# Performance work log

Hardware: AMD Instinct MI355X
Metric: run time of the kernel (lower is better)

The kernel has to match this reference:

```python
import jax, jax.numpy as jnp
import numpy as np

B, S, D_MODEL, D_K, D_V, H = 2, 2048, 1024, 1024, 1024, 16


def setup_inputs() -> dict:
    key = jax.random.key(0)
    ks = jax.random.split(key, 12)
    s = 0.02
    inp = {
        "queries": jax.random.normal(ks[0], (B, S, D_MODEL), jnp.float32),
        "keys": jax.random.normal(ks[1], (B, S, D_MODEL), jnp.float32),
        "values": jax.random.normal(ks[2], (B, S, D_MODEL), jnp.float32),
        # causal mask: 1 where attention is disallowed (added as -1e9*mask)
        "mask": jnp.triu(jnp.ones((1, 1, S, S), jnp.float32), k=1),
        "Wq": jax.random.normal(ks[3], (D_MODEL, D_K), jnp.float32) * s,
        "bq": jnp.zeros((D_K,), jnp.float32),
        "Wk": jax.random.normal(ks[4], (D_MODEL, D_K), jnp.float32) * s,
        "bk": jnp.zeros((D_K,), jnp.float32),
        "Wv": jax.random.normal(ks[5], (D_MODEL, D_V), jnp.float32) * s,
        "bv": jnp.zeros((D_V,), jnp.float32),
        "Wo": jax.random.normal(ks[6], (D_K, D_MODEL), jnp.float32) * s,
        "bo": jnp.zeros((D_MODEL,), jnp.float32),
    }
    return inp


def _split_heads(x):  # [B,S,D] -> [B,H,S,D/H]
    b, s, d = x.shape
    return x.reshape(b, s, H, d // H).transpose(0, 2, 1, 3)


def reference(queries, keys, values, mask, Wq, bq, Wk, bk, Wv, bv, Wo, bo):
    q = _split_heads(queries @ Wq + bq)   # [B,H,S,hd]
    k = _split_heads(keys @ Wk + bk)
    v = _split_heads(values @ Wv + bv)
    # NOTE: original scales by sqrt(full d_k), not per-head dim (faithful quirk)
    scores = jnp.einsum("bhqd,bhkd->bhqk", q, k) / jnp.sqrt(jnp.float32(D_K))
    scores = scores + (-1e9) * mask
    w = jax.nn.softmax(scores, axis=-1)
    out = jnp.einsum("bhqk,bhkd->bhqd", w, v)        # [B,H,S,hd]
    out = out.transpose(0, 2, 1, 3).reshape(q.shape[0], q.shape[2], D_K)
    return out @ Wo + bo
```

## Files before the change

### kernel.cpp

```cpp
#include <hip/hip_runtime.h>
#include <hip/hip_bf16.h>
#include <cstdint>

typedef __bf16 bf16;
typedef __bf16 bf16x2 __attribute__((ext_vector_type(2)));
typedef __bf16 bf16x4 __attribute__((ext_vector_type(4)));
typedef __bf16 bf16x8 __attribute__((ext_vector_type(8)));
typedef float f32x4 __attribute__((ext_vector_type(4)));
typedef float f32x16 __attribute__((ext_vector_type(16)));
typedef unsigned int u32;

#define B_ 2
#define S_ 2048
#define DM 1024
#define H_ 16
#define HD 64

__device__ __forceinline__ void gload_lds16(const bf16* g, bf16* l) {
  __builtin_amdgcn_global_load_lds((const __attribute__((address_space(1))) void*)g,
                                   (__attribute__((address_space(3))) void*)l,
                                   16, 0, 0);
}

__device__ __forceinline__ u32 cvt_pk_bf16(float lo, float hi) {
  u32 r;
  asm("v_cvt_pk_bf16_f32 %0, %1, %2" : "=v"(r) : "v"(lo), "v"(hi));
  return r;
}

__global__ __launch_bounds__(256) void convert_k(const float* __restrict__ s0,
                                                 const float* __restrict__ s1,
                                                 const float* __restrict__ s2,
                                                 bf16* __restrict__ d0,
                                                 bf16* __restrict__ d1,
                                                 bf16* __restrict__ d2) {
  const float* s = (blockIdx.z == 0) ? s0 : (blockIdx.z == 1) ? s1 : s2;
  bf16* d = (blockIdx.z == 0) ? d0 : (blockIdx.z == 1) ? d1 : d2;
  const size_t i = ((size_t)blockIdx.x * 256 + threadIdx.x) * 8;
  f32x4 a = *(const f32x4*)(s + i);
  f32x4 b = *(const f32x4*)(s + i + 4);
  bf16x8 o;
#pragma unroll
  for (int j = 0; j < 4; j++) { o[j] = (bf16)a[j]; o[j + 4] = (bf16)b[j]; }
  *(bf16x8*)(d + i) = o;
}

__global__ __launch_bounds__(256) void transposeW_k(
    const float* __restrict__ w0, const float* __restrict__ w1,
    const float* __restrict__ w2, const float* __restrict__ w3,
    bf16* __restrict__ t0, bf16* __restrict__ t1,
    bf16* __restrict__ t2, bf16* __restrict__ t3) {
  const float* src = (blockIdx.z == 0) ? w0 : (blockIdx.z == 1) ? w1
                     : (blockIdx.z == 2) ? w2 : w3;
  bf16* dst = (blockIdx.z == 0) ? t0 : (blockIdx.z == 1) ? t1
              : (blockIdx.z == 2) ? t2 : t3;
  __shared__ float tile[32][33];
  const int tx = threadIdx.x, ty = threadIdx.y;
  const int x0 = blockIdx.x * 32, y0 = blockIdx.y * 32;
#pragma unroll
  for (int r = 0; r < 4; r++)
    tile[ty + r * 8][tx] = src[(size_t)(y0 + ty + r * 8) * DM + x0 + tx];
  __syncthreads();
#pragma unroll
  for (int r = 0; r < 4; r++)
    dst[(size_t)(x0 + ty + r * 8) * DM + y0 + tx] = (bf16)tile[tx][ty + r * 8];
}

struct GArgs { const void* A; const bf16* Bt; const float* bias; void* C; };
struct GArgs3 { GArgs g[3]; };

__global__ __launch_bounds__(512, 1) void gemm128_k(GArgs3 args, int M, int N,
                                                    int K) {
  __shared__ __align__(16) bf16 SA_[73728];
  bf16* const SB_ = SA_ + 24576;

  const int nwg = gridDim.x;
  const int id = blockIdx.x;
  const int wgid = (id & 7) * (nwg >> 3) + (id >> 3);
  const int z = wgid >> 7;
  const int rem = wgid & 127;
  const int tx = rem >> 5, ty = rem & 31;
  const GArgs ga = args.g[z];
  const int m0 = ty * 128, n0 = tx * 256;

  const int tid = threadIdx.x;
  const int lane = tid & 63, w = tid >> 6;
  const int l15 = lane & 15, q = lane >> 4;
  const int wr = w >> 2, wc = w & 3;

  const bf16* gA[2];
  const bf16* gB[4];
  int dA[2], dB[4];
#pragma unroll
  for (int i = 0; i < 2; i++) {
    const int ci = i * 512 + w * 64 + lane;
    const int row = ci >> 3, sc = (ci & 7) ^ (row & 7);
    gA[i] = (const bf16*)ga.A + (size_t)(m0 + row) * K + sc * 8;
    dA[i] = (i * 512 + w * 64) * 8;
  }
#pragma unroll
  for (int i = 0; i < 4; i++) {
    const int ci = i * 512 + w * 64 + lane;
    const int row = ci >> 3, sc = (ci & 7) ^ (row & 7);
    gB[i] = ga.Bt + (size_t)(n0 + row) * K + sc * 8;
    dB[i] = (i * 512 + w * 64) * 8;
  }

  const int cA0 = (q ^ (l15 & 7)) * 8;
  const int cA1 = ((4 + q) ^ (l15 & 7)) * 8;

  f32x4 acc[4][4] = {};

  const int NT = K >> 6;

#pragma unroll
  for (int tt = 0; tt < 2; tt++) {
    bf16* Ab = SA_ + tt * 8192;
    bf16* Bb = SB_ + tt * 16384;
    const int k0 = tt * 64;
    gload_lds16(gA[0] + k0, Ab + dA[0]);
    gload_lds16(gA[1] + k0, Ab + dA[1]);
#pragma unroll
    for (int i = 0; i < 4; i++) gload_lds16(gB[i] + k0, Bb + dB[i]);
  }
  asm volatile("s_waitcnt vmcnt(6)" ::: "memory");
  __builtin_amdgcn_s_barrier();

  for (int t = 0; t < NT; ++t) {
    const int rb = t % 3;
    const int wb = (t + 2) % 3;
    const int kpre = ((t + 2 < NT) ? t + 2 : NT - 1) << 6;
    {
      bf16* Ab = SA_ + wb * 8192;
      bf16* Bb = SB_ + wb * 16384;
      gload_lds16(gA[0] + kpre, Ab + dA[0]);
      gload_lds16(gA[1] + kpre, Ab + dA[1]);
#pragma unroll
      for (int i = 0; i < 4; i++) gload_lds16(gB[i] + kpre, Bb + dB[i]);
    }

    const bf16* Ab = SA_ + rb * 8192;
    const bf16* Bb = SB_ + rb * 16384;
    bf16x8 a[4][2], b[4][2];
#pragma unroll
    for (int mt = 0; mt < 4; mt++) {
      const int ro = (wr * 64 + mt * 16 + l15) * 64;
      a[mt][0] = *(const bf16x8*)(Ab + ro + cA0);
      a[mt][1] = *(const bf16x8*)(Ab + ro + cA1);
    }
#pragma unroll
    for (int nt = 0; nt < 4; nt++) {
      const int ro = (wc * 64 + nt * 16 + l15) * 64;
      b[nt][0] = *(const bf16x8*)(Bb + ro + cA0);
      b[nt][1] = *(const bf16x8*)(Bb + ro + cA1);
    }

    __builtin_amdgcn_s_setprio(1);
#pragma unroll
    for (int mt = 0; mt < 4; mt++)
#pragma unroll
      for (int nt = 0; nt < 4; nt++)
#pragma unroll
        for (int kk = 0; kk < 2; kk++)
          acc[mt][nt] = __builtin_amdgcn_mfma_f32_16x16x32_bf16(
              a[mt][kk], b[nt][kk], acc[mt][nt], 0, 0, 0);
    __builtin_amdgcn_s_setprio(0);

    asm volatile("s_waitcnt vmcnt(6)" ::: "memory");
    __builtin_amdgcn_s_barrier();
  }

  asm volatile("s_waitcnt vmcnt(0)" ::: "memory");
  __builtin_amdgcn_s_barrier();

  bf16* Ws = SA_ + w * 4352;
#pragma unroll
  for (int nt = 0; nt < 4; nt++) {
    const float bv = ga.bias[n0 + wc * 64 + nt * 16 + l15];
#pragma unroll
    for (int mt = 0; mt < 4; mt++)
#pragma unroll
      for (int r = 0; r < 4; r++)
        Ws[(mt * 16 + q * 4 + r) * 68 + nt * 16 + l15] =
            (bf16)(acc[mt][nt][r] + bv);
  }
#pragma unroll
  for (int p = 0; p < 8; p++) {
    const int lr = p * 8 + (lane >> 3), c0 = (lane & 7) * 8;
    bf16x4 lo = *(const bf16x4*)(Ws + lr * 68 + c0);
    bf16x4 hi = *(const bf16x4*)(Ws + lr * 68 + c0 + 4);
    bf16x8 o;
#pragma unroll
    for (int j = 0; j < 4; j++) { o[j] = lo[j]; o[j + 4] = hi[j]; }
    *(bf16x8*)((bf16*)ga.C + (size_t)(m0 + wr * 64 + lr) * N + n0 + wc * 64 + c0) = o;
  }
}

__global__ __launch_bounds__(512, 1) void gemmo_k(const bf16* __restrict__ A,
                                                  const bf16* __restrict__ Bt,
                                                  const float* __restrict__ bias,
                                                  float* __restrict__ C,
                                                  int M, int N, int K) {
  __shared__ __align__(16) bf16 SA_[49152];
  bf16* const SB_ = SA_ + 24576;

  const int id = blockIdx.x;
  const int wgid = (id & 7) * 32 + (id >> 3);
  const int tx = wgid >> 5, ty = wgid & 31;
  const int m0 = ty * 128, n0 = tx * 128;

  const int tid = threadIdx.x;
  const int lane = tid & 63, w = tid >> 6;
  const int l15 = lane & 15, q = lane >> 4;
  const int wr = w >> 2, wc = w & 3;

  const bf16* gA[2];
  const bf16* gB[2];
  int dd[2];
#pragma unroll
  for (int i = 0; i < 2; i++) {
    const int ci = i * 512 + w * 64 + lane;
    const int row = ci >> 3, sc = (ci & 7) ^ (row & 7);
    gA[i] = A + (size_t)(m0 + row) * K + sc * 8;
    gB[i] = Bt + (size_t)(n0 + row) * K + sc * 8;
    dd[i] = ci * 8;
  }

  const int cA0 = (q ^ (l15 & 7)) * 8;
  const int cA1 = ((4 + q) ^ (l15 & 7)) * 8;

  f32x4 acc[4][2] = {};
  const int NT = K >> 6;

#pragma unroll
  for (int tt = 0; tt < 2; tt++) {
    const int k0 = tt * 64;
    gload_lds16(gA[0] + k0, SA_ + tt * 8192 + dd[0]);
    gload_lds16(gA[1] + k0, SA_ + tt * 8192 + dd[1]);
    gload_lds16(gB[0] + k0, SB_ + tt * 8192 + dd[0]);
    gload_lds16(gB[1] + k0, SB_ + tt * 8192 + dd[1]);
  }
  asm volatile("s_waitcnt vmcnt(4)" ::: "memory");
  __builtin_amdgcn_s_barrier();

  for (int t = 0; t < NT; ++t) {
    const int rb = t % 3;
    const int wb = (t + 2) % 3;
    const int kpre = ((t + 2 < NT) ? t + 2 : NT - 1) << 6;
    gload_lds16(gA[0] + kpre, SA_ + wb * 8192 + dd[0]);
    gload_lds16(gA[1] + kpre, SA_ + wb * 8192 + dd[1]);
    gload_lds16(gB[0] + kpre, SB_ + wb * 8192 + dd[0]);
    gload_lds16(gB[1] + kpre, SB_ + wb * 8192 + dd[1]);

    const bf16* Ab = SA_ + rb * 8192;
    const bf16* Bb = SB_ + rb * 8192;
    bf16x8 a[4][2], b[2][2];
#pragma unroll
    for (int mt = 0; mt < 4; mt++) {
      const int ro = (wr * 64 + mt * 16 + l15) * 64;
      a[mt][0] = *(const bf16x8*)(Ab + ro + cA0);
      a[mt][1] = *(const bf16x8*)(Ab + ro + cA1);
    }
#pragma unroll
    for (int nt = 0; nt < 2; nt++) {
      const int ro = (wc * 32 + nt * 16 + l15) * 64;
      b[nt][0] = *(const bf16x8*)(Bb + ro + cA0);
      b[nt][1] = *(const bf16x8*)(Bb + ro + cA1);
    }

    __builtin_amdgcn_s_setprio(1);
#pragma unroll
    for (int mt = 0; mt < 4; mt++)
#pragma unroll
      for (int nt = 0; nt < 2; nt++)
#pragma unroll
        for (int kk = 0; kk < 2; kk++)
          acc[mt][nt] = __builtin_amdgcn_mfma_f32_16x16x32_bf16(
              a[mt][kk], b[nt][kk], acc[mt][nt], 0, 0, 0);
    __builtin_amdgcn_s_setprio(0);

    asm volatile("s_waitcnt vmcnt(4)" ::: "memory");
    __builtin_amdgcn_s_barrier();
  }

  asm volatile("s_waitcnt vmcnt(0)" ::: "memory");
  __builtin_amdgcn_s_barrier();

  float* Ws = (float*)SA_ + w * 2304;
#pragma unroll
  for (int nt = 0; nt < 2; nt++) {
    const float bv = bias[n0 + wc * 32 + nt * 16 + l15];
#pragma unroll
    for (int mt = 0; mt < 4; mt++)
#pragma unroll
      for (int r = 0; r < 4; r++)
        Ws[(mt * 16 + q * 4 + r) * 36 + nt * 16 + l15] = acc[mt][nt][r] + bv;
  }
#pragma unroll
  for (int p = 0; p < 8; p++) {
    const int lr = p * 8 + (lane >> 3), c0 = (lane & 7) * 4;
    f32x4 v = *(const f32x4*)(Ws + lr * 36 + c0);
    *(f32x4*)(C + (size_t)(m0 + wr * 64 + lr) * N + n0 + wc * 32 + c0) = v;
  }
}

template <bool AF32, bool CF32>
__global__ __launch_bounds__(256) void gemm_k(GArgs3 args, int M, int N, int K) {
  const GArgs ga = args.g[blockIdx.z];
  __shared__ __align__(16) bf16 As[128 * 32];
  __shared__ __align__(16) bf16 Bs[128 * 32];
  const int tid = threadIdx.x;
  const int lane = tid & 63, w = tid >> 6;
  const int l15 = lane & 15, q = lane >> 4;
  const int wr = w >> 1, wc = w & 1;
  const int m0 = blockIdx.y * 128, n0 = blockIdx.x * 128;

  const int c0 = w * 128 + lane;
  const int c1 = c0 + 64;
  const int r0 = c0 >> 2, r1 = c1 >> 2, koff = (c0 & 3) * 8;
  const bf16* gB0 = ga.Bt + (size_t)(n0 + r0) * K + koff;
  const bf16* gB1 = ga.Bt + (size_t)(n0 + r1) * K + koff;
  bf16* lA0 = As + (w * 2 + 0) * 512;
  bf16* lA1 = As + (w * 2 + 1) * 512;
  bf16* lB0 = Bs + (w * 2 + 0) * 512;
  bf16* lB1 = Bs + (w * 2 + 1) * 512;

  const float* pA0 = nullptr;
  const float* pA1 = nullptr;
  f32x4 t00, t01, t10, t11;
  if constexpr (AF32) {
    const float* A = (const float*)ga.A;
    pA0 = A + (size_t)(m0 + r0) * K + koff;
    pA1 = A + (size_t)(m0 + r1) * K + koff;
    t00 = *(const f32x4*)pA0; t01 = *(const f32x4*)(pA0 + 4);
    t10 = *(const f32x4*)pA1; t11 = *(const f32x4*)(pA1 + 4);
  }

  f32x4 acc[4][4] = {};

  for (int k0 = 0; k0 < K; k0 += 32) {
    if constexpr (AF32) {
      bf16x8 va0, va1;
#pragma unroll
      for (int j = 0; j < 4; j++) {
        va0[j] = (bf16)t00[j]; va0[j + 4] = (bf16)t01[j];
        va1[j] = (bf16)t10[j]; va1[j + 4] = (bf16)t11[j];
      }
      *(bf16x8*)(lA0 + lane * 8) = va0;
      *(bf16x8*)(lA1 + lane * 8) = va1;
    } else {
      const bf16* A = (const bf16*)ga.A;
      gload_lds16(A + (size_t)(m0 + r0) * K + koff + k0, lA0);
      gload_lds16(A + (size_t)(m0 + r1) * K + koff + k0, lA1);
    }
    gload_lds16(gB0 + k0, lB0);
    gload_lds16(gB1 + k0, lB1);
    __syncthreads();

    bf16x8 a[4], b[4];
#pragma unroll
    for (int mt = 0; mt < 4; mt++)
      a[mt] = *(const bf16x8*)(As + (wr * 64 + mt * 16 + l15) * 32 + q * 8);
#pragma unroll
    for (int nt = 0; nt < 4; nt++)
      b[nt] = *(const bf16x8*)(Bs + (wc * 64 + nt * 16 + l15) * 32 + q * 8);

    if constexpr (AF32) {
      const int kn = (k0 + 32 < K) ? k0 + 32 : k0;
      t00 = *(const f32x4*)(pA0 + kn); t01 = *(const f32x4*)(pA0 + kn + 4);
      t10 = *(const f32x4*)(pA1 + kn); t11 = *(const f32x4*)(pA1 + kn + 4);
    }

#pragma unroll
    for (int mt = 0; mt < 4; mt++)
#pragma unroll
      for (int nt = 0; nt < 4; nt++)
        acc[mt][nt] = __builtin_amdgcn_mfma_f32_16x16x32_bf16(a[mt], b[nt],
                                                              acc[mt][nt], 0, 0, 0);
    __syncthreads();
  }

#pragma unroll
  for (int nt = 0; nt < 4; nt++) {
    const int col = n0 + wc * 64 + nt * 16 + l15;
    const float bv = ga.bias[col];
#pragma unroll
    for (int mt = 0; mt < 4; mt++) {
      const int row = m0 + wr * 64 + mt * 16 + q * 4;
#pragma unroll
      for (int r = 0; r < 4; r++) {
        const float val = acc[mt][nt][r] + bv;
        if constexpr (CF32)
          ((float*)ga.C)[(size_t)(row + r) * N + col] = val;
        else
          ((bf16*)ga.C)[(size_t)(row + r) * N + col] = (bf16)val;
      }
    }
  }
}

__global__ __launch_bounds__(512, 4) void attn_k(const bf16* __restrict__ Qp,
                                                 const bf16* __restrict__ Kp,
                                                 const bf16* __restrict__ Vp,
                                                 bf16* __restrict__ Op) {
  const int g = blockIdx.x;
  const int xcd = g & 7, s = g >> 3;
  const int gl = s & 3, tau = s >> 2;
  const int bh = xcd * 4 + gl;
  const int b = bh >> 4, h = bh & 15;
  const int xt = (tau < 8) ? tau : 23 - tau;
  const int i0 = xt * 128;
  const int NI = 2 * xt + 2;

  const int tid = threadIdx.x;
  const int lane = tid & 63, w = tid >> 6;
  const int l31 = lane & 31, hi = lane >> 5;
  const int qq = w >> 1, kh = w & 1;

  __shared__ __align__(16) char smem[33792];
  bf16 (*Ks)[64][64] = (bf16 (*)[64][64])smem;
  bf16 (*Vts)[64][64] = (bf16 (*)[64][64])(smem + 16384);

  const size_t headoff = (size_t)b * S_ * DM + h * HD;
  const bf16* Kb = Kp + headoff;
  const bf16* Vb = Vp + headoff;

  const int kr = tid >> 3, kcb = (tid & 7) * 8;
  const int cK = ((tid & 7) ^ (kr & 7)) * 8;
  const int d0 = (tid & 31) * 2, kq = (tid >> 5) * 4;
  const int cV0 = ((kq >> 3) ^ (d0 & 7)) * 8 + (kq & 7);
  const int cV1 = ((kq >> 3) ^ ((d0 + 1) & 7)) * 8 + (kq & 7);
  const float QSCALE = 0.04508422f;

  bf16x8 qreg[4];
  {
    const bf16* qb = Qp + headoff + (size_t)(i0 + qq * 32 + l31) * DM + hi * 8;
#pragma unroll
    for (int kk = 0; kk < 4; kk++) {
      bf16x8 v = *(const bf16x8*)(qb + kk * 16);
      bf16x8 o;
#pragma unroll
      for (int j = 0; j < 8; j++) o[j] = (bf16)((float)v[j] * QSCALE);
      qreg[kk] = o;
    }
  }

  bf16x8 kR = *(const bf16x8*)(Kb + (size_t)kr * DM + kcb);
  bf16x2 vR[4];
#pragma unroll
  for (int j = 0; j < 4; j++)
    vR[j] = *(const bf16x2*)(Vb + (size_t)(kq + j) * DM + d0);
  *(bf16x8*)&Ks[0][kr][cK] = kR;
  {
    bf16x4 vlo, vhi;
#pragma unroll
    for (int j = 0; j < 4; j++) { vlo[j] = vR[j][0]; vhi[j] = vR[j][1]; }
    *(bf16x4*)&Vts[0][d0][cV0] = vlo;
    *(bf16x4*)&Vts[0][d0 + 1][cV1] = vhi;
  }
  kR = *(const bf16x8*)(Kb + (size_t)(64 + kr) * DM + kcb);
#pragma unroll
  for (int j = 0; j < 4; j++)
    vR[j] = *(const bf16x2*)(Vb + (size_t)(64 + kq + j) * DM + d0);
  __syncthreads();

  f32x16 oacc0 = {}, oacc1 = {};
  float rsum = 0.f;
  int buf = 0;
  const int qbase = i0 + qq * 32;

  for (int t = 0; t < NI; ++t, buf ^= 1) {
    if (t + 1 < NI) {
      *(bf16x8*)&Ks[buf ^ 1][kr][cK] = kR;
      bf16x4 vlo, vhi;
#pragma unroll
      for (int j = 0; j < 4; j++) { vlo[j] = vR[j][0]; vhi[j] = vR[j][1]; }
      *(bf16x4*)&Vts[buf ^ 1][d0][cV0] = vlo;
      *(bf16x4*)&Vts[buf ^ 1][d0 + 1][cV1] = vhi;
    }
    if (t + 2 < NI) {
      const size_t jn = (size_t)(t + 2) * 64;
      kR = *(const bf16x8*)(Kb + (jn + kr) * DM + kcb);
#pragma unroll
      for (int j = 0; j < 4; j++)
        vR[j] = *(const bf16x2*)(Vb + (jn + kq + j) * DM + d0);
    }

    const int kbase = t * 64 + kh * 32;
    if (kbase <= qbase + 31) {
      f32x16 sa = {}, sb = {};
      __builtin_amdgcn_s_setprio(1);
#pragma unroll
      for (int kk = 0; kk < 2; kk++) {
        bf16x8 ka = *(const bf16x8*)
            &Ks[buf][kh * 32 + l31][((2 * kk + hi) ^ (l31 & 7)) * 8];
        sa = __builtin_amdgcn_mfma_f32_32x32x16_bf16(ka, qreg[kk], sa, 0, 0, 0);
      }
#pragma unroll
      for (int kk = 2; kk < 4; kk++) {
        bf16x8 ka = *(const bf16x8*)
            &Ks[buf][kh * 32 + l31][((2 * kk + hi) ^ (l31 & 7)) * 8];
        sb = __builtin_amdgcn_mfma_f32_32x32x16_bf16(ka, qreg[kk], sb, 0, 0, 0);
      }
      __builtin_amdgcn_s_setprio(0);

      float p[16];
      if (kbase + 31 > qbase) {
        const int qrl = qbase + l31;
#pragma unroll
        for (int r = 0; r < 16; r++) {
          const int keyl = kbase + (r & 3) + 8 * (r >> 2) + 4 * hi;
          p[r] = (keyl <= qrl) ? __builtin_amdgcn_exp2f(sa[r] + sb[r]) : 0.f;
        }
      } else {
#pragma unroll
        for (int r = 0; r < 16; r++)
          p[r] = __builtin_amdgcn_exp2f(sa[r] + sb[r]);
      }
      {
        float q0 = (p[0] + p[1]) + (p[2] + p[3]);
        float q1 = (p[4] + p[5]) + (p[6] + p[7]);
        float q2 = (p[8] + p[9]) + (p[10] + p[11]);
        float q3 = (p[12] + p[13]) + (p[14] + p[15]);
        rsum += (q0 + q1) + (q2 + q3);
      }

      u32 Aq[4][2];
#pragma unroll
      for (int t2 = 0; t2 < 4; t2++) {
        Aq[t2][0] = cvt_pk_bf16(p[4 * t2 + 0], p[4 * t2 + 1]);
        Aq[t2][1] = cvt_pk_bf16(p[4 * t2 + 2], p[4 * t2 + 3]);
      }
      bf16x8 pb[2];
#pragma unroll
      for (int s2 = 0; s2 < 2; s2++) {
        auto e0 = __builtin_amdgcn_permlane32_swap(Aq[2 * s2][0], Aq[2 * s2 + 1][0], false, false);
        auto e1 = __builtin_amdgcn_permlane32_swap(Aq[2 * s2][1], Aq[2 * s2 + 1][1], false, false);
        union { u32 u[4]; bf16x8 v; } cv;
        cv.u[0] = e0[0]; cv.u[1] = e1[0]; cv.u[2] = e0[1]; cv.u[3] = e1[1];
        pb[s2] = cv.v;
      }

      __builtin_amdgcn_s_setprio(1);
#pragma unroll
      for (int s2 = 0; s2 < 2; s2++) {
        const int cv = ((kh * 4 + s2 * 2 + hi) ^ (l31 & 7)) * 8;
        bf16x8 va0 = *(const bf16x8*)&Vts[buf][l31][cv];
        bf16x8 va1 = *(const bf16x8*)&Vts[buf][32 + l31][cv];
        oacc0 = __builtin_amdgcn_mfma_f32_32x32x16_bf16(va0, pb[s2], oacc0, 0, 0, 0);
        oacc1 = __builtin_amdgcn_mfma_f32_32x32x16_bf16(va1, pb[s2], oacc1, 0, 0, 0);
      }
      __builtin_amdgcn_s_setprio(0);
    }

    __syncthreads();
  }

  float rtot_w = rsum + __shfl_xor(rsum, 32);
  float* osum = (float*)smem;
  float* auxf = (float*)(smem + 32768);
  if (kh == 0) {
#pragma unroll
    for (int m = 0; m < 2; m++)
#pragma unroll
      for (int rq = 0; rq < 4; rq++) {
        f32x4 v4;
#pragma unroll
        for (int e = 0; e < 4; e++)
          v4[e] = m ? oacc1[rq * 4 + e] : oacc0[rq * 4 + e];
        *(f32x4*)(osum + qq * 2048 + (m * 4 + rq) * 256 + lane * 4) = v4;
      }
  }
  if (lane < 32) auxf[w * 32 + lane] = rtot_w;
  __syncthreads();
  if (kh == 1) {
#pragma unroll
    for (int m = 0; m < 2; m++)
#pragma unroll
      for (int rq = 0; rq < 4; rq++) {
        float* pp = osum + qq * 2048 + (m * 4 + rq) * 256 + lane * 4;
        f32x4 v4 = *(f32x4*)pp;
#pragma unroll
        for (int e = 0; e < 4; e++)
          v4[e] += m ? oacc1[rq * 4 + e] : oacc0[rq * 4 + e];
        *(f32x4*)pp = v4;
      }
  }
  __syncthreads();

  {
    const int q = tid >> 2, q31b = q & 31, qq2 = q >> 5;
    const float rtot = auxf[(qq2 * 2 + 0) * 32 + q31b] + auxf[(qq2 * 2 + 1) * 32 + q31b];
    const float rinv = 1.0f / rtot;
    const int dbase = (tid & 3) * 16;
    bf16* orow = Op + headoff + (size_t)(i0 + q) * DM + dbase;
#pragma unroll
    for (int gg = 0; gg < 2; gg++) {
      bf16x8 o8;
#pragma unroll
      for (int e = 0; e < 8; e++) {
        const int d = dbase + gg * 8 + e;
        const int base = (((d >> 5) << 2) | ((d >> 3) & 3)) * 256 +
                         (q31b + 32 * ((d >> 2) & 1)) * 4 + (d & 3);
        o8[e] = (bf16)(osum[qq2 * 2048 + base] * rinv);
      }
      *(bf16x8*)(orow + gg * 8) = o8;
    }
  }
}

extern "C" void kernel_launch(void* const* d_in, const int* in_sizes, int n_in,
                              void* d_out, int out_size, void* d_ws, size_t ws_size,
                              hipStream_t stream) {
  const float* q_in = (const float*)d_in[0];
  const float* k_in = (const float*)d_in[1];
  const float* v_in = (const float*)d_in[2];
  const float* Wq = (const float*)d_in[4];
  const float* bq = (const float*)d_in[5];
  const float* Wk = (const float*)d_in[6];
  const float* bk = (const float*)d_in[7];
  const float* Wv = (const float*)d_in[8];
  const float* bv = (const float*)d_in[9];
  const float* Wo = (const float*)d_in[10];
  const float* bo = (const float*)d_in[11];

  bf16* ws = (bf16*)d_ws;
  const size_t NQ = (size_t)B_ * S_ * DM;
  bf16* Qp = ws;
  bf16* Kp = ws + NQ;
  bf16* Vp = ws + 2 * NQ;
  bf16* WqT = ws + 3 * NQ;
  bf16* WkT = WqT + (size_t)DM * DM;
  bf16* WvT = WkT + (size_t)DM * DM;
  bf16* WoT = WvT + (size_t)DM * DM;
  bf16* qb = WoT + (size_t)DM * DM;
  bf16* kb = qb + NQ;
  bf16* vb = kb + NQ;

  const bool fast = ws_size >= (size_t)(28 * 1024 * 1024) * 2;

  transposeW_k<<<dim3(32, 32, 4), dim3(32, 8), 0, stream>>>(
      Wq, Wk, Wv, Wo, WqT, WkT, WvT, WoT);

  if (fast) {
    convert_k<<<dim3((B_ * S_ * DM) / (256 * 8), 1, 3), 256, 0, stream>>>(
        q_in, k_in, v_in, qb, kb, vb);
    GArgs3 g3;
    g3.g[0] = {qb, WqT, bq, Qp};
    g3.g[1] = {kb, WkT, bk, Kp};
    g3.g[2] = {vb, WvT, bv, Vp};
    gemm128_k<<<dim3(384), 512, 0, stream>>>(g3, B_ * S_, DM, DM);
  } else {
    GArgs3 g3;
    g3.g[0] = {q_in, WqT, bq, Qp};
    g3.g[1] = {k_in, WkT, bk, Kp};
    g3.g[2] = {v_in, WvT, bv, Vp};
    gemm_k<true, false><<<dim3(DM / 128, (B_ * S_) / 128, 3), 256, 0, stream>>>(
        g3, B_ * S_, DM, DM);
  }

  attn_k<<<dim3(512, 1, 1), 512, 0, stream>>>(Qp, Kp, Vp, Qp);

  gemmo_k<<<dim3(256), 512, 0, stream>>>(Qp, WoT, bo, (float*)d_out,
                                         B_ * S_, DM, DM);
}
```

Baseline: 216.6 us.

## Fuse fp32-to-bf16 input conversion into the QKV projection GEMM

Removes the separate convert_k pass that wrote bf16 copies of queries/keys/values. The GEMM now loads fp32 A tiles into registers three stages ahead, converts them to bf16 and stores them into swizzled LDS, while B keeps using direct global-to-LDS loads. This avoids a full read/write round trip of the activations and one launch, but doubles A global read bytes inside the GEMM and adds register pressure and VALU conversion work in the main loop. The fallback gemm_k path is deleted.

```diff
diff --git a/kernel.cpp b/kernel.cpp
--- a/kernel.cpp
+++ b/kernel.cpp
@@ -28,21 +28,11 @@
   return r;
 }
 
-__global__ __launch_bounds__(256) void convert_k(const float* __restrict__ s0,
-                                                 const float* __restrict__ s1,
-                                                 const float* __restrict__ s2,
-                                                 bf16* __restrict__ d0,
-                                                 bf16* __restrict__ d1,
-                                                 bf16* __restrict__ d2) {
-  const float* s = (blockIdx.z == 0) ? s0 : (blockIdx.z == 1) ? s1 : s2;
-  bf16* d = (blockIdx.z == 0) ? d0 : (blockIdx.z == 1) ? d1 : d2;
-  const size_t i = ((size_t)blockIdx.x * 256 + threadIdx.x) * 8;
-  f32x4 a = *(const f32x4*)(s + i);
-  f32x4 b = *(const f32x4*)(s + i + 4);
+__device__ __forceinline__ bf16x8 cvt8(f32x4 lo, f32x4 hi) {
   bf16x8 o;
 #pragma unroll
-  for (int j = 0; j < 4; j++) { o[j] = (bf16)a[j]; o[j + 4] = (bf16)b[j]; }
-  *(bf16x8*)(d + i) = o;
+  for (int j = 0; j < 4; j++) { o[j] = (bf16)lo[j]; o[j + 4] = (bf16)hi[j]; }
+  return o;
 }
 
 __global__ __launch_bounds__(256) void transposeW_k(
@@ -88,16 +78,17 @@
   const int l15 = lane & 15, q = lane >> 4;
   const int wr = w >> 2, wc = w & 3;
 
-  const bf16* gA[2];
-  const bf16* gB[4];
-  int dA[2], dB[4];
+  const float* gAf[2];
+  int dAwr[2];
 #pragma unroll
   for (int i = 0; i < 2; i++) {
     const int ci = i * 512 + w * 64 + lane;
     const int row = ci >> 3, sc = (ci & 7) ^ (row & 7);
-    gA[i] = (const bf16*)ga.A + (size_t)(m0 + row) * K + sc * 8;
-    dA[i] = (i * 512 + w * 64) * 8;
-  }
+    gAf[i] = (const float*)ga.A + (size_t)(m0 + row) * K + sc * 8;
+    dAwr[i] = ci * 8;
+  }
+  const bf16* gB[4];
+  int dB[4];
 #pragma unroll
   for (int i = 0; i < 4; i++) {
     const int ci = i * 512 + w * 64 + lane;
@@ -110,34 +101,43 @@
   const int cA1 = ((4 + q) ^ (l15 & 7)) * 8;
 
   f32x4 acc[4][4] = {};
-
   const int NT = K >> 6;
 
-#pragma unroll
-  for (int tt = 0; tt < 2; tt++) {
-    bf16* Ab = SA_ + tt * 8192;
-    bf16* Bb = SB_ + tt * 16384;
-    const int k0 = tt * 64;
-    gload_lds16(gA[0] + k0, Ab + dA[0]);
-    gload_lds16(gA[1] + k0, Ab + dA[1]);
-#pragma unroll
-    for (int i = 0; i < 4; i++) gload_lds16(gB[i] + k0, Bb + dB[i]);
-  }
-  asm volatile("s_waitcnt vmcnt(6)" ::: "memory");
+  f32x4 a0l = *(const f32x4*)(gAf[0]);
+  f32x4 a0h = *(const f32x4*)(gAf[0] + 4);
+  f32x4 a1l = *(const f32x4*)(gAf[1]);
+  f32x4 a1h = *(const f32x4*)(gAf[1] + 4);
+  f32x4 c0l = *(const f32x4*)(gAf[0] + 64);
+  f32x4 c0h = *(const f32x4*)(gAf[0] + 68);
+  f32x4 c1l = *(const f32x4*)(gAf[1] + 64);
+  f32x4 c1h = *(const f32x4*)(gAf[1] + 68);
+#pragma unroll
+  for (int i = 0; i < 4; i++) gload_lds16(gB[i], SB_ + dB[i]);
+  f32x4 p0l = *(const f32x4*)(gAf[0] + 128);
+  f32x4 p0h = *(const f32x4*)(gAf[0] + 132);
+  f32x4 p1l = *(const f32x4*)(gAf[1] + 128);
+  f32x4 p1h = *(const f32x4*)(gAf[1] + 132);
+#pragma unroll
+  for (int i = 0; i < 4; i++) gload_lds16(gB[i] + 64, SB_ + 16384 + dB[i]);
+  *(bf16x8*)(SA_ + dAwr[0]) = cvt8(a0l, a0h);
+  *(bf16x8*)(SA_ + dAwr[1]) = cvt8(a1l, a1h);
+  *(bf16x8*)(SA_ + 8192 + dAwr[0]) = cvt8(c0l, c0h);
+  *(bf16x8*)(SA_ + 8192 + dAwr[1]) = cvt8(c1l, c1h);
+  asm volatile("s_waitcnt vmcnt(8) lgkmcnt(0)" ::: "memory");
   __builtin_amdgcn_s_barrier();
 
   for (int t = 0; t < NT; ++t) {
     const int rb = t % 3;
-    const int wb = (t + 2) % 3;
-    const int kpre = ((t + 2 < NT) ? t + 2 : NT - 1) << 6;
-    {
-      bf16* Ab = SA_ + wb * 8192;
-      bf16* Bb = SB_ + wb * 16384;
-      gload_lds16(gA[0] + kpre, Ab + dA[0]);
-      gload_lds16(gA[1] + kpre, Ab + dA[1]);
-#pragma unroll
-      for (int i = 0; i < 4; i++) gload_lds16(gB[i] + kpre, Bb + dB[i]);
-    }
+    const int w2 = (t + 2) % 3;
+    *(bf16x8*)(SA_ + w2 * 8192 + dAwr[0]) = cvt8(p0l, p0h);
+    *(bf16x8*)(SA_ + w2 * 8192 + dAwr[1]) = cvt8(p1l, p1h);
+    const int ka = ((t + 3 < NT) ? t + 3 : NT - 1) << 6;
+    p0l = *(const f32x4*)(gAf[0] + ka); p0h = *(const f32x4*)(gAf[0] + ka + 4);
+    p1l = *(const f32x4*)(gAf[1] + ka); p1h = *(const f32x4*)(gAf[1] + ka + 4);
+    const int kb2 = ((t + 2 < NT) ? t + 2 : NT - 1) << 6;
+#pragma unroll
+    for (int i = 0; i < 4; i++)
+      gload_lds16(gB[i] + kb2, SB_ + w2 * 16384 + dB[i]);
 
     const bf16* Ab = SA_ + rb * 8192;
     const bf16* Bb = SB_ + rb * 16384;
@@ -154,7 +154,6 @@
       b[nt][0] = *(const bf16x8*)(Bb + ro + cA0);
       b[nt][1] = *(const bf16x8*)(Bb + ro + cA1);
     }
-
     __builtin_amdgcn_s_setprio(1);
 #pragma unroll
     for (int mt = 0; mt < 4; mt++)
@@ -166,11 +165,11 @@
               a[mt][kk], b[nt][kk], acc[mt][nt], 0, 0, 0);
     __builtin_amdgcn_s_setprio(0);
 
-    asm volatile("s_waitcnt vmcnt(6)" ::: "memory");
+    asm volatile("s_waitcnt vmcnt(8) lgkmcnt(0)" ::: "memory");
     __builtin_amdgcn_s_barrier();
   }
 
-  asm volatile("s_waitcnt vmcnt(0)" ::: "memory");
+  asm volatile("s_waitcnt vmcnt(0) lgkmcnt(0)" ::: "memory");
   __builtin_amdgcn_s_barrier();
 
   bf16* Ws = SA_ + w * 4352;
@@ -301,101 +300,6 @@
     const int lr = p * 8 + (lane >> 3), c0 = (lane & 7) * 4;
     f32x4 v = *(const f32x4*)(Ws + lr * 36 + c0);
     *(f32x4*)(C + (size_t)(m0 + wr * 64 + lr) * N + n0 + wc * 32 + c0) = v;
-  }
-}
-
-template <bool AF32, bool CF32>
-__global__ __launch_bounds__(256) void gemm_k(GArgs3 args, int M, int N, int K) {
-  const GArgs ga = args.g[blockIdx.z];
-  __shared__ __align__(16) bf16 As[128 * 32];
-  __shared__ __align__(16) bf16 Bs[128 * 32];
-  const int tid = threadIdx.x;
-  const int lane = tid & 63, w = tid >> 6;
-  const int l15 = lane & 15, q = lane >> 4;
-  const int wr = w >> 1, wc = w & 1;
-  const int m0 = blockIdx.y * 128, n0 = blockIdx.x * 128;
-
-  const int c0 = w * 128 + lane;
-  const int c1 = c0 + 64;
-  const int r0 = c0 >> 2, r1 = c1 >> 2, koff = (c0 & 3) * 8;
-  const bf16* gB0 = ga.Bt + (size_t)(n0 + r0) * K + koff;
-  const bf16* gB1 = ga.Bt + (size_t)(n0 + r1) * K + koff;
-  bf16* lA0 = As + (w * 2 + 0) * 512;
-  bf16* lA1 = As + (w * 2 + 1) * 512;
-  bf16* lB0 = Bs + (w * 2 + 0) * 512;
-  bf16* lB1 = Bs + (w * 2 + 1) * 512;
-
-  const float* pA0 = nullptr;
-  const float* pA1 = nullptr;
-  f32x4 t00, t01, t10, t11;
-  if constexpr (AF32) {
-    const float* A = (const float*)ga.A;
-    pA0 = A + (size_t)(m0 + r0) * K + koff;
-    pA1 = A + (size_t)(m0 + r1) * K + koff;
-    t00 = *(const f32x4*)pA0; t01 = *(const f32x4*)(pA0 + 4);
-    t10 = *(const f32x4*)pA1; t11 = *(const f32x4*)(pA1 + 4);
-  }
-
-  f32x4 acc[4][4] = {};
-
-  for (int k0 = 0; k0 < K; k0 += 32) {
-    if constexpr (AF32) {
-      bf16x8 va0, va1;
-#pragma unroll
-      for (int j = 0; j < 4; j++) {
-        va0[j] = (bf16)t00[j]; va0[j + 4] = (bf16)t01[j];
-        va1[j] = (bf16)t10[j]; va1[j + 4] = (bf16)t11[j];
-      }
-      *(bf16x8*)(lA0 + lane * 8) = va0;
-      *(bf16x8*)(lA1 + lane * 8) = va1;
-    } else {
-      const bf16* A = (const bf16*)ga.A;
-      gload_lds16(A + (size_t)(m0 + r0) * K + koff + k0, lA0);
-      gload_lds16(A + (size_t)(m0 + r1) * K + koff + k0, lA1);
-    }
-    gload_lds16(gB0 + k0, lB0);
-    gload_lds16(gB1 + k0, lB1);
-    __syncthreads();
-
-    bf16x8 a[4], b[4];
-#pragma unroll
-    for (int mt = 0; mt < 4; mt++)
-      a[mt] = *(const bf16x8*)(As + (wr * 64 + mt * 16 + l15) * 32 + q * 8);
-#pragma unroll
-    for (int nt = 0; nt < 4; nt++)
-      b[nt] = *(const bf16x8*)(Bs + (wc * 64 + nt * 16 + l15) * 32 + q * 8);
-
-    if constexpr (AF32) {
-      const int kn = (k0 + 32 < K) ? k0 + 32 : k0;
-      t00 = *(const f32x4*)(pA0 + kn); t01 = *(const f32x4*)(pA0 + kn + 4);
-      t10 = *(const f32x4*)(pA1 + kn); t11 = *(const f32x4*)(pA1 + kn + 4);
-    }
-
-#pragma unroll
-    for (int mt = 0; mt < 4; mt++)
-#pragma unroll
-      for (int nt = 0; nt < 4; nt++)
-        acc[mt][nt] = __builtin_amdgcn_mfma_f32_16x16x32_bf16(a[mt], b[nt],
-                                                              acc[mt][nt], 0, 0, 0);
-    __syncthreads();
-  }
-
-#pragma unroll
-  for (int nt = 0; nt < 4; nt++) {
-    const int col = n0 + wc * 64 + nt * 16 + l15;
-    const float bv = ga.bias[col];
-#pragma unroll
-    for (int mt = 0; mt < 4; mt++) {
-      const int row = m0 + wr * 64 + mt * 16 + q * 4;
-#pragma unroll
-      for (int r = 0; r < 4; r++) {
-        const float val = acc[mt][nt][r] + bv;
-        if constexpr (CF32)
-          ((float*)ga.C)[(size_t)(row + r) * N + col] = val;
-        else
-          ((bf16*)ga.C)[(size_t)(row + r) * N + col] = (bf16)val;
-      }
-    }
   }
 }
 
@@ -633,31 +537,15 @@
   bf16* WkT = WqT + (size_t)DM * DM;
   bf16* WvT = WkT + (size_t)DM * DM;
   bf16* WoT = WvT + (size_t)DM * DM;
-  bf16* qb = WoT + (size_t)DM * DM;
-  bf16* kb = qb + NQ;
-  bf16* vb = kb + NQ;
-
-  const bool fast = ws_size >= (size_t)(28 * 1024 * 1024) * 2;
 
   transposeW_k<<<dim3(32, 32, 4), dim3(32, 8), 0, stream>>>(
       Wq, Wk, Wv, Wo, WqT, WkT, WvT, WoT);
 
-  if (fast) {
-    convert_k<<<dim3((B_ * S_ * DM) / (256 * 8), 1, 3), 256, 0, stream>>>(
-        q_in, k_in, v_in, qb, kb, vb);
-    GArgs3 g3;
-    g3.g[0] = {qb, WqT, bq, Qp};
-    g3.g[1] = {kb, WkT, bk, Kp};
-    g3.g[2] = {vb, WvT, bv, Vp};
-    gemm128_k<<<dim3(384), 512, 0, stream>>>(g3, B_ * S_, DM, DM);
-  } else {
-    GArgs3 g3;
-    g3.g[0] = {q_in, WqT, bq, Qp};
-    g3.g[1] = {k_in, WkT, bk, Kp};
-    g3.g[2] = {v_in, WvT, bv, Vp};
-    gemm_k<true, false><<<dim3(DM / 128, (B_ * S_) / 128, 3), 256, 0, stream>>>(
-        g3, B_ * S_, DM, DM);
-  }
+  GArgs3 g3;
+  g3.g[0] = {q_in, WqT, bq, Qp};
+  g3.g[1] = {k_in, WkT, bk, Kp};
+  g3.g[2] = {v_in, WvT, bv, Vp};
+  gemm128_k<<<dim3(384), 512, 0, stream>>>(g3, B_ * S_, DM, DM);
 
   attn_k<<<dim3(512, 1, 1), 512, 0, stream>>>(Qp, Kp, Vp, Qp);
 
```

Result: faster. 210.7 us (-2.7%).
